# Kernel tuning notes

Measured on AMD Instinct MI355X. Metric: run time of the kernel, lower is better.

Reference implementation:

```python
import jax, jax.numpy as jnp
import numpy as np

C_M, C_Z, C_H = 256, 128, 32
EPS = 1e-3
LN_EPS = 1e-5


def setup_inputs() -> dict:
    key = jax.random.key(0)
    ks = jax.random.split(key, 10)
    S, R = 128, 256
    inp = {
        'm_1': jax.random.normal(ks[0], (S, R, C_M), jnp.float32),
        'm_2': jax.random.normal(ks[1], (S, R, C_M), jnp.float32),
        'mask_1': jnp.ones((S, R), jnp.float32),
        'mask_2': jnp.ones((S, R), jnp.float32),
        # LayerNorm params
        'ln1_w': jnp.ones((C_M,), jnp.float32),
        'ln1_b': jnp.zeros((C_M,), jnp.float32),
        'ln2_w': jnp.ones((C_M,), jnp.float32),
        'ln2_b': jnp.zeros((C_M,), jnp.float32),
        # Linear params
        'w1': jax.random.normal(ks[2], (C_M, C_H), jnp.float32) * (1.0 / np.sqrt(C_M)),
        'b1': jnp.zeros((C_H,), jnp.float32),
        'w2': jax.random.normal(ks[3], (C_M, C_H), jnp.float32) * (1.0 / np.sqrt(C_M)),
        'b2': jnp.zeros((C_H,), jnp.float32),
        'w_out': jax.random.normal(ks[4], (C_H * C_H, C_Z), jnp.float32) * 0.02,
        'b_out': jnp.zeros((C_Z,), jnp.float32),
    }
    return inp


def _layer_norm(x, w, b):
    mu = jnp.mean(x, axis=-1, keepdims=True)
    var = jnp.mean(jnp.square(x - mu), axis=-1, keepdims=True)
    return (x - mu) * jax.lax.rsqrt(var + LN_EPS) * w + b


def reference(m_1, m_2, mask_1, mask_2, ln1_w, ln1_b, ln2_w, ln2_b,
              w1, b1, w2, b2, w_out, b_out):
    # m_*: [S, R, C_M]; mask_*: [S, R]
    a = (_layer_norm(m_1, ln1_w, ln1_b) @ w1 + b1) * mask_1[..., None]  # [S,R,H]
    b = (_layer_norm(m_2, ln2_w, ln2_b) @ w2 + b2) * mask_2[..., None]  # [S,R,H]
    # outer product mean over sequence dim: [R, R, H, H]
    outer = jnp.einsum('sic,sje->ijce', a, b)
    S, R, H = a.shape
    outer = outer.reshape(R, R, H * H)
    z = outer @ w_out + b_out  # [R, R, C_Z]
    norm = jnp.einsum('si,sj->ij', mask_1, mask_2)[..., None] + EPS  # [R,R,1]
    return z / norm
```

## Files before the change

kernel.cpp:

```cpp
#include <hip/hip_runtime.h>
#include <hip/hip_bf16.h>

#define S_DIM 128
#define R_DIM 256
#define CM    256
#define H_DIM 32
#define CZ    128

typedef short s8v   __attribute__((ext_vector_type(8)));
typedef float f32x4 __attribute__((ext_vector_type(4)));
typedef float f32x16 __attribute__((ext_vector_type(16)));
using bf16 = __hip_bfloat16;

static __device__ __forceinline__ unsigned short bf16_bits(float f) {
  return __builtin_bit_cast(unsigned short, __float2bfloat16(f));
}

static __device__ __forceinline__ void gload_lds16(const void* g, void* l) {
  __builtin_amdgcn_global_load_lds(
      (const __attribute__((address_space(1))) unsigned int*)g,
      (__attribute__((address_space(3))) unsigned int*)l, 16, 0, 0);
}

__global__ __launch_bounds__(256) void opm_prep(
    const float* __restrict__ w_out,
    const float* __restrict__ mask1, const float* __restrict__ mask2,
    const float* __restrict__ w1, const float* __restrict__ w2,
    bf16* __restrict__ wT2, float* __restrict__ rnorm, bf16* __restrict__ wF)
{
  const int b   = blockIdx.x;
  const int tid = threadIdx.x;
  if (b < 64) {
    const int vid  = b*256 + tid;
    const int lane = vid & 63;
    const int ks2  = (vid >> 6) & 63;
    const int tb   = vid >> 12;
    const int t    = tb*32 + (lane & 31);
    const int hf   = lane >> 5;
    unsigned int pk[4];
    #pragma unroll
    for (int ep = 0; ep < 4; ++ep) {
      const int ce0 = ks2*16 + hf*8 + ep*2;
      const int ce1 = ce0 + 1;
      unsigned int w0 = bf16_bits(w_out[((ce0 & 31)*32 + (ce0 >> 5))*CZ + t]);
      unsigned int w1b = bf16_bits(w_out[((ce1 & 31)*32 + (ce1 >> 5))*CZ + t]);
      pk[ep] = w0 | (w1b << 16);
    }
    uint4 o = {pk[0], pk[1], pk[2], pk[3]};
    *reinterpret_cast<uint4*>((char*)wT2 + (size_t)vid*16) = o;
  } else if (b < 320) {
    const int i = b - 64;
    const int j = tid;
    float acc = 0.f;
    for (int s = 0; s < S_DIM; ++s)
      acc += mask1[(size_t)s*R_DIM + i] * mask2[(size_t)s*R_DIM + j];
    rnorm[i*R_DIM + j] = 1.0f / (acc + 1e-3f);
  } else {
    const int mat = b - 320;
    const float* __restrict__ w = mat ? w2 : w1;
    bf16* __restrict__ dst = wF + mat*8192;
    #pragma unroll
    for (int it = 0; it < 4; ++it) {
      const int vid  = it*256 + tid;
      const int nf   = vid >> 9;
      const int ks   = (vid >> 6) & 7;
      const int lane = vid & 63;
      const int h    = nf*16 + (lane & 15);
      unsigned int pk[4];
      #pragma unroll
      for (int ep = 0; ep < 4; ++ep) {
        const int c0 = ks*32 + (lane >> 4)*8 + ep*2;
        unsigned int lo = bf16_bits(w[c0*H_DIM + h]);
        unsigned int hi = bf16_bits(w[(c0 + 1)*H_DIM + h]);
        pk[ep] = lo | (hi << 16);
      }
      uint4 o = {pk[0], pk[1], pk[2], pk[3]};
      *reinterpret_cast<uint4*>((char*)dst + (size_t)vid*16) = o;
    }
  }
}

__global__ __launch_bounds__(64) void opm_proj(
    const float* __restrict__ m1, const float* __restrict__ m2,
    const float* __restrict__ ln1w, const float* __restrict__ ln1b,
    const float* __restrict__ ln2w, const float* __restrict__ ln2b,
    const float* __restrict__ b1, const float* __restrict__ b2,
    const float* __restrict__ mask1, const float* __restrict__ mask2,
    const bf16* __restrict__ wF, bf16* __restrict__ aT, bf16* __restrict__ bT)
{
  __shared__ char xn[8192];

  const int mat = blockIdx.y;
  const float* __restrict__ m    = mat ? m2   : m1;
  const float* __restrict__ lnw  = mat ? ln2w : ln1w;
  const float* __restrict__ lnb  = mat ? ln2b : ln1b;
  const float* __restrict__ bias = mat ? b2   : b1;
  const float* __restrict__ mask = mat ? mask2 : mask1;
  const bf16* __restrict__ wf    = wF + mat*8192;
  bf16* __restrict__ dst         = mat ? bT   : aT;

  const int lane = threadIdx.x;
  const int row  = lane & 15;
  const int q    = lane >> 4;
  const int r    = blockIdx.x & 255;
  const int sb   = blockIdx.x >> 8;
  const int s    = sb*16 + row;

  const float4* __restrict__ src =
      reinterpret_cast<const float4*>(m + ((size_t)s*R_DIM + r)*CM + q*64);
  float4 x[16];
  float sum = 0.f, sq = 0.f;
  #pragma unroll
  for (int i = 0; i < 16; ++i) {
    x[i] = src[i];
    sum += x[i].x + x[i].y + x[i].z + x[i].w;
    sq  += x[i].x*x[i].x + x[i].y*x[i].y + x[i].z*x[i].z + x[i].w*x[i].w;
  }
  sum += __shfl_xor(sum, 16); sum += __shfl_xor(sum, 32);
  sq  += __shfl_xor(sq, 16);  sq  += __shfl_xor(sq, 32);
  const float mu = sum * (1.0f/CM);
  const float rs = rsqrtf(sq * (1.0f/CM) - mu*mu + 1e-5f);

  const float4* __restrict__ lw4 = reinterpret_cast<const float4*>(lnw + q*64);
  const float4* __restrict__ lb4 = reinterpret_cast<const float4*>(lnb + q*64);
  #pragma unroll
  for (int i2 = 0; i2 < 8; ++i2) {
    unsigned int pk[4];
    #pragma unroll
    for (int half = 0; half < 2; ++half) {
      const int i = i2*2 + half;
      const float4 lw = lw4[i];
      const float4 lb = lb4[i];
      const float v0 = (x[i].x - mu)*rs*lw.x + lb.x;
      const float v1 = (x[i].y - mu)*rs*lw.y + lb.y;
      const float v2 = (x[i].z - mu)*rs*lw.z + lb.z;
      const float v3 = (x[i].w - mu)*rs*lw.w + lb.w;
      pk[half*2+0] = (unsigned)bf16_bits(v0) | ((unsigned)bf16_bits(v1) << 16);
      pk[half*2+1] = (unsigned)bf16_bits(v2) | ((unsigned)bf16_bits(v3) << 16);
    }
    int off = row*512 + q*128 + i2*16;
    off ^= (row & 7) << 4;
    uint4 o = {pk[0], pk[1], pk[2], pk[3]};
    *reinterpret_cast<uint4*>(xn + off) = o;
  }
  __syncthreads();

  const float bv0 = bias[row];
  const float bv1 = bias[16 + row];
  f32x4 z0 = {bv0, bv0, bv0, bv0};
  f32x4 z1 = {bv1, bv1, bv1, bv1};
  #pragma unroll
  for (int ks = 0; ks < 8; ++ks) {
    int off = row*512 + ks*64 + q*16;
    off ^= (row & 7) << 4;
    const s8v a  = *reinterpret_cast<const s8v*>(xn + off);
    const s8v w0 = *reinterpret_cast<const s8v*>((const char*)wf + (ks*64 + lane)*16);
    const s8v w1 = *reinterpret_cast<const s8v*>((const char*)wf + ((8 + ks)*64 + lane)*16);
    z0 = __builtin_amdgcn_mfma_f32_16x16x32_bf16(a, w0, z0, 0, 0, 0);
    z1 = __builtin_amdgcn_mfma_f32_16x16x32_bf16(a, w1, z1, 0, 0, 0);
  }

  float mk[4];
  #pragma unroll
  for (int rr = 0; rr < 4; ++rr)
    mk[rr] = mask[(size_t)(sb*16 + q*4 + rr)*R_DIM + r];

  unsigned int pa0 = (unsigned)bf16_bits(z0[0]*mk[0]) | ((unsigned)bf16_bits(z0[1]*mk[1]) << 16);
  unsigned int pa1 = (unsigned)bf16_bits(z0[2]*mk[2]) | ((unsigned)bf16_bits(z0[3]*mk[3]) << 16);
  unsigned int pb0 = (unsigned)bf16_bits(z1[0]*mk[0]) | ((unsigned)bf16_bits(z1[1]*mk[1]) << 16);
  unsigned int pb1 = (unsigned)bf16_bits(z1[2]*mk[2]) | ((unsigned)bf16_bits(z1[3]*mk[3]) << 16);

  const int p0 = r*H_DIM + row;
  const int p1 = r*H_DIM + 16 + row;
  const int c0 = sb*2 + (q >> 1);
  const int rem = (q & 1) * 8;
  {
    uint2 v; v.x = pa0; v.y = pa1;
    *reinterpret_cast<uint2*>((char*)dst + (size_t)p0*256 + ((c0 ^ (p0 & 7)) << 4) + rem) = v;
  }
  {
    uint2 v; v.x = pb0; v.y = pb1;
    *reinterpret_cast<uint2*>((char*)dst + (size_t)p1*256 + ((c0 ^ (p1 & 7)) << 4) + rem) = v;
  }
}

__global__ __launch_bounds__(512, 2) void opm_gemm(
    const bf16* __restrict__ aT, const bf16* __restrict__ bT,
    const bf16* __restrict__ wT2, const float* __restrict__ b_out,
    const float* __restrict__ rnorm, float* __restrict__ out)
{
  __shared__ char smem[131072];

  const int tid  = threadIdx.x;
  const int lane = tid & 63;
  const int wid  = tid >> 6;
  const int l31  = lane & 31;
  const int hf   = lane >> 5;

  int swz = blockIdx.x;
  swz = (swz & 7)*128 + (swz >> 3);
  const int bx = swz >> 5, by = swz & 31;

  {
    const char* gA = (const char*)aT + (size_t)bx*65536;
    const char* gB = (const char*)bT + (size_t)by*65536;
    #pragma unroll
    for (int i = 0; i < 8; ++i) {
      const int base = (i*8 + wid)*1024;
      gload_lds16(gA + base + lane*16, smem + base);
      gload_lds16(gB + base + lane*16, smem + 65536 + base);
    }
  }
  __syncthreads();

  const int wm = wid >> 2, wn = wid & 3;
  f32x16 acc[4][2];
  #pragma unroll
  for (int mf = 0; mf < 4; ++mf)
    #pragma unroll
    for (int nf = 0; nf < 2; ++nf)
      #pragma unroll
      for (int r = 0; r < 16; ++r) acc[mf][nf][r] = 0.f;

  #pragma unroll
  for (int ks = 0; ks < 8; ++ks) {
    s8v af[4], bfv[2];
    #pragma unroll
    for (int mf = 0; mf < 4; ++mf) {
      const int mm = wm*128 + mf*32 + l31;
      int L = mm*256 + ks*32 + hf*16;
      L ^= (mm & 7) << 4;
      af[mf] = *reinterpret_cast<const s8v*>(smem + L);
    }
    #pragma unroll
    for (int nf = 0; nf < 2; ++nf) {
      const int nn = wn*64 + nf*32 + l31;
      int L = nn*256 + ks*32 + hf*16;
      L ^= (nn & 7) << 4;
      bfv[nf] = *reinterpret_cast<const s8v*>(smem + 65536 + L);
    }
    #pragma unroll
    for (int mf = 0; mf < 4; ++mf)
      #pragma unroll
      for (int nf = 0; nf < 2; ++nf)
        acc[mf][nf] = __builtin_amdgcn_mfma_f32_32x32x16_bf16(af[mf], bfv[nf], acc[mf][nf], 0, 0, 0);
  }
  __syncthreads();

  #pragma unroll
  for (int mf = 0; mf < 4; ++mf) {
    #pragma unroll
    for (int nf = 0; nf < 2; ++nf) {
      const int pair = (wm*4 + mf)*8 + wn*2 + nf;
      #pragma unroll
      for (int g = 0; g < 4; ++g) {
        const unsigned int lo = (unsigned)bf16_bits(acc[mf][nf][4*g+0]) |
                                ((unsigned)bf16_bits(acc[mf][nf][4*g+1]) << 16);
        const unsigned int hi = (unsigned)bf16_bits(acc[mf][nf][4*g+2]) |
                                ((unsigned)bf16_bits(acc[mf][nf][4*g+3]) << 16);
        const int L0 = pair*2048 + (l31*32 + 8*g + 4*hf)*2;
        const int L  = L0 ^ ((((pair & 7) ^ ((L0 >> 7) & 7))) << 4);
        uint2 v; v.x = lo; v.y = hi;
        *reinterpret_cast<uint2*>(smem + L) = v;
      }
    }
  }
  __syncthreads();

  {
    const int pm = wid >> 2, pn = wid & 3;
    const int t  = pn*32 + l31;
    const float bo = b_out[t];
    f32x16 ze, zo;
    #pragma unroll
    for (int r = 0; r < 16; ++r) { ze[r] = bo; zo[r] = 0.f; }

    const char* wb = (const char*)wT2 + ((size_t)(pn*64)*64 + lane)*16;
    const int pair = pm*32 + l31;
    #pragma unroll 8
    for (int ks2 = 0; ks2 < 64; ++ks2) {
      const s8v bw = *reinterpret_cast<const s8v*>(wb + ks2*1024);
      int L0 = pair*2048 + ks2*32 + hf*16;
      int L  = L0 ^ ((((pair & 7) ^ ((L0 >> 7) & 7))) << 4);
      const s8v a = *reinterpret_cast<const s8v*>(smem + L);
      if (ks2 & 1)
        zo = __builtin_amdgcn_mfma_f32_32x32x16_bf16(a, bw, zo, 0, 0, 0);
      else
        ze = __builtin_amdgcn_mfma_f32_32x32x16_bf16(a, bw, ze, 0, 0, 0);
    }

    #pragma unroll
    for (int r = 0; r < 16; ++r) {
      const float z = ze[r] + zo[r];
      const int row = (r & 3) + 8*(r >> 2) + 4*hf;
      const int pr  = pm*32 + row;
      const int o   = (bx*8 + (pr >> 3))*R_DIM + by*8 + (pr & 7);
      out[(size_t)o*CZ + t] = z * rnorm[o];
    }
  }
}

extern "C" void kernel_launch(void* const* d_in, const int* in_sizes, int n_in,
                              void* d_out, int out_size, void* d_ws, size_t ws_size,
                              hipStream_t stream) {
  const float* m_1    = (const float*)d_in[0];
  const float* m_2    = (const float*)d_in[1];
  const float* mask_1 = (const float*)d_in[2];
  const float* mask_2 = (const float*)d_in[3];
  const float* ln1_w  = (const float*)d_in[4];
  const float* ln1_b  = (const float*)d_in[5];
  const float* ln2_w  = (const float*)d_in[6];
  const float* ln2_b  = (const float*)d_in[7];
  const float* w1     = (const float*)d_in[8];
  const float* b1     = (const float*)d_in[9];
  const float* w2     = (const float*)d_in[10];
  const float* b2     = (const float*)d_in[11];
  const float* w_out  = (const float*)d_in[12];
  const float* b_out  = (const float*)d_in[13];
  float* out = (float*)d_out;

  char* ws = (char*)d_ws;
  bf16* aT    = (bf16*)ws;
  bf16* bT    = (bf16*)(ws + (2u << 20));
  bf16* wT2   = (bf16*)(ws + (4u << 20));
  float* rnrm = (float*)(ws + (4u << 20) + (256u << 10));
  bf16* wF    = (bf16*)(ws + (4u << 20) + (512u << 10));

  opm_prep<<<dim3(322),      dim3(256), 0, stream>>>(w_out, mask_1, mask_2,
      w1, w2, wT2, rnrm, wF);
  opm_proj<<<dim3(2048, 2),  dim3(64),  0, stream>>>(m_1, m_2, ln1_w, ln1_b,
      ln2_w, ln2_b, b1, b2, mask_1, mask_2, wF, aT, bT);
  opm_gemm<<<dim3(1024),     dim3(512), 0, stream>>>(aT, bT, wT2, b_out, rnrm, out);
}
```

Measured before the change: 77.45 us.

## Widen LDS XOR swizzle and split second GEMM along K across warps

The LDS XOR swizzle is widened from 8 to 16 chunk positions in the prep store, the main GEMM fragment loads and the bf16 staging of the outer product, to cut bank conflicts. The second GEMM (outer product times w_out) is reorganised so each warp covers both 32-row pair groups over half of K. Each w_out fragment load now feeds two MFMAs. The two K halves are then summed through LDS before the output is written, which costs an extra barrier and an LDS round trip, and only half the warps do the epilogue.

```diff
diff --git a/kernel.cpp b/kernel.cpp
--- a/kernel.cpp
+++ b/kernel.cpp
@@ -176,11 +176,11 @@
   const int rem = (q & 1) * 8;
   {
     uint2 v; v.x = pa0; v.y = pa1;
-    *reinterpret_cast<uint2*>((char*)dst + (size_t)p0*256 + ((c0 ^ (p0 & 7)) << 4) + rem) = v;
+    *reinterpret_cast<uint2*>((char*)dst + (size_t)p0*256 + ((c0 ^ (p0 & 15)) << 4) + rem) = v;
   }
   {
     uint2 v; v.x = pb0; v.y = pb1;
-    *reinterpret_cast<uint2*>((char*)dst + (size_t)p1*256 + ((c0 ^ (p1 & 7)) << 4) + rem) = v;
+    *reinterpret_cast<uint2*>((char*)dst + (size_t)p1*256 + ((c0 ^ (p1 & 15)) << 4) + rem) = v;
   }
 }
 
@@ -228,15 +228,13 @@
     #pragma unroll
     for (int mf = 0; mf < 4; ++mf) {
       const int mm = wm*128 + mf*32 + l31;
-      int L = mm*256 + ks*32 + hf*16;
-      L ^= (mm & 7) << 4;
+      int L = (mm*256 + ks*32 + hf*16) ^ ((mm & 15) << 4);
       af[mf] = *reinterpret_cast<const s8v*>(smem + L);
     }
     #pragma unroll
     for (int nf = 0; nf < 2; ++nf) {
       const int nn = wn*64 + nf*32 + l31;
-      int L = nn*256 + ks*32 + hf*16;
-      L ^= (nn & 7) << 4;
+      int L = (nn*256 + ks*32 + hf*16) ^ ((nn & 15) << 4);
       bfv[nf] = *reinterpret_cast<const s8v*>(smem + 65536 + L);
     }
     #pragma unroll
@@ -259,7 +257,7 @@
         const unsigned int hi = (unsigned)bf16_bits(acc[mf][nf][4*g+2]) |
                                 ((unsigned)bf16_bits(acc[mf][nf][4*g+3]) << 16);
         const int L0 = pair*2048 + (l31*32 + 8*g + 4*hf)*2;
-        const int L  = L0 ^ ((((pair & 7) ^ ((L0 >> 7) & 7))) << 4);
+        const int L  = L0 ^ ((((pair & 15) ^ ((L0 >> 7) & 15))) << 4);
         uint2 v; v.x = lo; v.y = hi;
         *reinterpret_cast<uint2*>(smem + L) = v;
       }
@@ -267,35 +265,70 @@
   }
   __syncthreads();
 
-  {
-    const int pm = wid >> 2, pn = wid & 3;
-    const int t  = pn*32 + l31;
-    const float bo = b_out[t];
-    f32x16 ze, zo;
-    #pragma unroll
-    for (int r = 0; r < 16; ++r) { ze[r] = bo; zo[r] = 0.f; }
-
-    const char* wb = (const char*)wT2 + ((size_t)(pn*64)*64 + lane)*16;
-    const int pair = pm*32 + l31;
+  const int kh = wid >> 2, pn = wid & 3;
+  const int t  = pn*32 + l31;
+  f32x16 z0, z1;
+  {
+    const float init = (kh == 0) ? b_out[t] : 0.f;
+    #pragma unroll
+    for (int r = 0; r < 16; ++r) { z0[r] = init; z1[r] = init; }
+  }
+  {
+    const char* wb = (const char*)wT2 + ((size_t)(pn*64 + kh*32)*64 + lane)*16;
     #pragma unroll 8
-    for (int ks2 = 0; ks2 < 64; ++ks2) {
-      const s8v bw = *reinterpret_cast<const s8v*>(wb + ks2*1024);
-      int L0 = pair*2048 + ks2*32 + hf*16;
-      int L  = L0 ^ ((((pair & 7) ^ ((L0 >> 7) & 7))) << 4);
-      const s8v a = *reinterpret_cast<const s8v*>(smem + L);
-      if (ks2 & 1)
-        zo = __builtin_amdgcn_mfma_f32_32x32x16_bf16(a, bw, zo, 0, 0, 0);
-      else
-        ze = __builtin_amdgcn_mfma_f32_32x32x16_bf16(a, bw, ze, 0, 0, 0);
-    }
-
+    for (int ks = 0; ks < 32; ++ks) {
+      const int ks2 = kh*32 + ks;
+      const s8v bw = *reinterpret_cast<const s8v*>(wb + ks*1024);
+      {
+        const int pair = l31;
+        int L0 = pair*2048 + ks2*32 + hf*16;
+        int L  = L0 ^ ((((pair & 15) ^ ((L0 >> 7) & 15))) << 4);
+        const s8v a = *reinterpret_cast<const s8v*>(smem + L);
+        z0 = __builtin_amdgcn_mfma_f32_32x32x16_bf16(a, bw, z0, 0, 0, 0);
+      }
+      {
+        const int pair = 32 + l31;
+        int L0 = pair*2048 + ks2*32 + hf*16;
+        int L  = L0 ^ ((((pair & 15) ^ ((L0 >> 7) & 15))) << 4);
+        const s8v a = *reinterpret_cast<const s8v*>(smem + L);
+        z1 = __builtin_amdgcn_mfma_f32_32x32x16_bf16(a, bw, z1, 0, 0, 0);
+      }
+    }
+  }
+  __syncthreads();
+
+  if (kh == 1) {
+    #pragma unroll
+    for (int g = 0; g < 4; ++g) {
+      f32x4 v0 = {z0[4*g+0], z0[4*g+1], z0[4*g+2], z0[4*g+3]};
+      f32x4 v1 = {z1[4*g+0], z1[4*g+1], z1[4*g+2], z1[4*g+3]};
+      *reinterpret_cast<f32x4*>(smem + pn*16384 +        g*1024 + lane*16) = v0;
+      *reinterpret_cast<f32x4*>(smem + pn*16384 + 8192 + g*1024 + lane*16) = v1;
+    }
+  }
+  __syncthreads();
+
+  if (kh == 0) {
+    #pragma unroll
+    for (int g = 0; g < 4; ++g) {
+      const f32x4 p0 = *reinterpret_cast<const f32x4*>(smem + pn*16384 +        g*1024 + lane*16);
+      const f32x4 p1 = *reinterpret_cast<const f32x4*>(smem + pn*16384 + 8192 + g*1024 + lane*16);
+      #pragma unroll
+      for (int j = 0; j < 4; ++j) { z0[4*g+j] += p0[j]; z1[4*g+j] += p1[j]; }
+    }
     #pragma unroll
     for (int r = 0; r < 16; ++r) {
-      const float z = ze[r] + zo[r];
       const int row = (r & 3) + 8*(r >> 2) + 4*hf;
-      const int pr  = pm*32 + row;
-      const int o   = (bx*8 + (pr >> 3))*R_DIM + by*8 + (pr & 7);
-      out[(size_t)o*CZ + t] = z * rnorm[o];
+      {
+        const int pr = row;
+        const int o  = (bx*8 + (pr >> 3))*R_DIM + by*8 + (pr & 7);
+        out[(size_t)o*CZ + t] = z0[r] * rnorm[o];
+      }
+      {
+        const int pr = 32 + row;
+        const int o  = (bx*8 + (pr >> 3))*R_DIM + by*8 + (pr & 7);
+        out[(size_t)o*CZ + t] = z1[r] * rnorm[o];
+      }
     }
   }
 }
```

Result: faster. 74.53 us (-3.8%).
